# Performance work log

Hardware: AMD Instinct MI355X
Metric: run time of the kernel (lower is better)

The kernel has to match this reference:

```python
import jax, jax.numpy as jnp
import numpy as np

RING_SIZES = list(range(3, 27, 2))  # 3,5,...,25 -> 12 rings; (1+12)*96 = 1248
BN_EPS = 1e-5


def _box_sum(x, k):
    """Sum over k x k window (k odd), 'same' zero padding. x: [B,C,H,W].
    O(1) per pixel via summed-area table instead of dense depthwise conv."""
    p = k // 2
    H, W = x.shape[2], x.shape[3]
    xp = jnp.pad(x, ((0, 0), (0, 0), (p, p), (p, p)))
    S = jnp.cumsum(jnp.cumsum(xp, axis=2), axis=3)
    S = jnp.pad(S, ((0, 0), (0, 0), (1, 0), (1, 0)))  # leading zero row/col
    return (S[:, :, k:k + H, k:k + W] - S[:, :, :H, k:k + W]
            - S[:, :, k:k + H, :W] + S[:, :, :H, :W])


def _ring_sum(x, k):
    """Depthwise conv with a k x k ring of ones == box(k) - box(k-2)."""
    inner = x if k == 3 else _box_sum(x, k - 2)
    return _box_sum(x, k) - inner


def _bn_eval(x, gamma, beta, mean, var):
    scale = gamma / jnp.sqrt(var + BN_EPS)
    return x * scale[None, :, None, None] + (beta - mean * scale)[None, :, None, None]


def _conv1x1(x, w, b):
    # x: [B,C,H,W], w: [O,C] -> [B,O,H,W]
    return jnp.einsum('bchw,oc->bohw', x, w) + b[None, :, None, None]


def setup_inputs() -> dict:
    key = jax.random.key(0)
    ks = jax.random.split(key, 13)
    B, C, H, W = 4, 96, 128, 128
    return {
        'x': jax.random.normal(ks[0], (B, C, H, W), jnp.float32),
        'bn1_gamma': jax.random.uniform(ks[1], (1248,), jnp.float32, 0.5, 1.5),
        'bn1_beta': jax.random.normal(ks[2], (1248,), jnp.float32) * 0.1,
        'bn1_mean': jax.random.normal(ks[3], (1248,), jnp.float32),
        'bn1_var': jax.random.uniform(ks[4], (1248,), jnp.float32, 0.5, 1.5),
        'conv1_w': jax.random.normal(ks[5], (512, 1248), jnp.float32) * (1.0 / np.sqrt(1248)),
        'conv1_b': jax.random.normal(ks[6], (512,), jnp.float32) * 0.01,
        'bn2_gamma': jax.random.uniform(ks[7], (512,), jnp.float32, 0.5, 1.5),
        'bn2_beta': jax.random.normal(ks[8], (512,), jnp.float32) * 0.1,
        'bn2_mean': jax.random.normal(ks[9], (512,), jnp.float32),
        'bn2_var': jax.random.uniform(ks[10], (512,), jnp.float32, 0.5, 1.5),
        'conv2_w': jax.random.normal(ks[11], (96, 512), jnp.float32) * (1.0 / np.sqrt(512)),
        'conv2_b': jax.random.normal(ks[12], (96,), jnp.float32) * 0.01,
    }


def reference(x, bn1_gamma, bn1_beta, bn1_mean, bn1_var, conv1_w, conv1_b,
              bn2_gamma, bn2_beta, bn2_mean, bn2_var, conv2_w, conv2_b):
    convs = [x] + [_ring_sum(x, k) for k in RING_SIZES]
    h = jnp.concatenate(convs, axis=1)  # [B, 1248, H, W]
    h = _bn_eval(h, bn1_gamma, bn1_beta, bn1_mean, bn1_var)
    h = jax.nn.relu(_conv1x1(h, conv1_w, conv1_b))
    h = _bn_eval(h, bn2_gamma, bn2_beta, bn2_mean, bn2_var)
    return _conv1x1(h, conv2_w, conv2_b)
```

## Files before the change

### kernel.cpp

```cpp
#include <hip/hip_runtime.h>
#include <hip/hip_bf16.h>
#include <cstdint>

typedef __attribute__((ext_vector_type(8))) short bf16x8;
typedef __attribute__((ext_vector_type(4))) float f32x4;

#define BN_EPS 1e-5f

__global__ __launch_bounds__(256) void prep1_kernel(
    const float* __restrict__ W1, const float* __restrict__ cb1,
    const float* __restrict__ g1, const float* __restrict__ be1,
    const float* __restrict__ mu1, const float* __restrict__ va1,
    __hip_bfloat16* __restrict__ V, float* __restrict__ b1e)
{
  int o = blockIdx.x;
  int t = threadIdx.x;
  const float* wrow = W1 + (size_t)o * 1248;
  float acc = 0.f;
  for (int i = t; i < 1248; i += 256) {
    float s = g1[i] * rsqrtf(va1[i] + BN_EPS);
    float w = wrow[i];
    acc += w * (be1[i] - mu1[i] * s);
    float g = w * s;
    float gn = 0.f;
    if (i < 1152) {
      float sn = g1[i + 96] * rsqrtf(va1[i + 96] + BN_EPS);
      gn = wrow[i + 96] * sn;
    }
    V[(size_t)o * 1248 + i] = __float2bfloat16(g - gn);
  }
  for (int d = 32; d > 0; d >>= 1) acc += __shfl_down(acc, d);
  __shared__ float red[4];
  int lane = t & 63, wv = t >> 6;
  if (lane == 0) red[wv] = acc;
  __syncthreads();
  if (t == 0) b1e[o] = cb1[o] + red[0] + red[1] + red[2] + red[3];
}

__global__ __launch_bounds__(256) void prep2_kernel(
    const float* __restrict__ W2, const float* __restrict__ cb2,
    const float* __restrict__ g2, const float* __restrict__ be2,
    const float* __restrict__ mu2, const float* __restrict__ va2,
    __hip_bfloat16* __restrict__ W2e, float* __restrict__ b2e)
{
  int o = blockIdx.x;
  int t = threadIdx.x;
  const float* wrow = W2 + (size_t)o * 512;
  float acc = 0.f;
  for (int j = t; j < 512; j += 256) {
    float s = g2[j] * rsqrtf(va2[j] + BN_EPS);
    float wv = wrow[j];
    acc += wv * (be2[j] - mu2[j] * s);
    W2e[(size_t)o * 512 + j] = __float2bfloat16(wv * s);
  }
  for (int d = 32; d > 0; d >>= 1) acc += __shfl_down(acc, d);
  __shared__ float red[4];
  int lane = t & 63, wv2 = t >> 6;
  if (lane == 0) red[wv2] = acc;
  __syncthreads();
  if (t == 0) b2e[o] = cb2[o] + red[0] + red[1] + red[2] + red[3];
}

__global__ __launch_bounds__(128) void sat_kernel(
    const float* __restrict__ x, float* __restrict__ SAT)
{
  int plane = blockIdx.x;
  const float* xp = x + (size_t)plane * 16384;
  __shared__ float tile[16384];
  int t = threadIdx.x;
  for (int i4 = t; i4 < 4096; i4 += 128) {
    int r = i4 >> 5;
    int g = i4 & 31;
    float4 v = *(const float4*)(xp + (size_t)r * 128 + g * 4);
    *(float4*)(tile + r * 128 + ((g ^ (r & 31)) << 2)) = v;
  }
  __syncthreads();
  {
    int r = t;
    float carry = 0.f;
    for (int g = 0; g < 32; ++g) {
      float* p = tile + r * 128 + ((g ^ (r & 31)) << 2);
      float4 v = *(float4*)p;
      float s0 = carry + v.x, s1 = s0 + v.y, s2 = s1 + v.z, s3 = s2 + v.w;
      float4 o; o.x = s0; o.y = s1; o.z = s2; o.w = s3;
      *(float4*)p = o;
      carry = s3;
    }
  }
  __syncthreads();
  float* Sg = SAT + (size_t)plane * 17028;
  Sg[t] = 0.f;
  if (t < 4) Sg[128 + t] = 0.f;
  Sg[(t + 1) * 132] = 0.f;
  int gc = t >> 2, wc = t & 3;
  float run = 0.f;
  for (int r = 0; r < 128; ++r) {
    run += tile[r * 128 + ((gc ^ (r & 31)) << 2) + wc];
    Sg[(r + 1) * 132 + t + 1] = run;
  }
}

__global__ __launch_bounds__(1024) void fused1_kernel(
    const float* __restrict__ SAT, const __hip_bfloat16* __restrict__ V,
    const float* __restrict__ b1e, const __hip_bfloat16* __restrict__ W2e,
    const float* __restrict__ b2e, float* __restrict__ out, int nb, int b0)
{
  extern __shared__ __align__(16) char smem[];
  float* E = (float*)smem;
  __hip_bfloat16* As = (__hip_bfloat16*)(smem + 50688);

  int blk = blockIdx.x;
  int rows_per_xcd = (nb * 128) >> 3;
  int r = (blk & 7) * rows_per_xcd + (blk >> 3);
  int bL = r >> 7, y = r & 127;

  int t = threadIdx.x;
  int lane = t & 63, wv = t >> 6;
  int wm = wv & 1, wn = wv >> 1;
  int lr = lane & 15, quad = lane >> 4;
  int px = t & 127;
  int bg = t >> 7;

  const float* Sb = SAT + (size_t)bL * 96 * 17028;

  f32x4 acc[4][4];
#pragma unroll
  for (int i = 0; i < 4; ++i)
#pragma unroll
    for (int jn = 0; jn < 4; ++jn) acc[i][jn] = (f32x4){0.f, 0.f, 0.f, 0.f};

  auto efill = [&](int j) {
    int y1 = (y - j < 0) ? 0 : (y - j);
    int y2 = ((y + j > 127) ? 127 : (y + j)) + 1;
    for (int idx = t; idx < 3168; idx += 1024) {
      int cl = idx / 33;
      int ck = idx - cl * 33;
      const float* bp = Sb + (size_t)cl * 17028 + ck * 4;
      float4 a = *(const float4*)(bp + y2 * 132);
      float4 b = *(const float4*)(bp + y1 * 132);
      float4 d;
      d.x = a.x - b.x; d.y = a.y - b.y; d.z = a.z - b.z; d.w = a.w - b.w;
      *(float4*)(E + cl * 132 + ck * 4) = d;
    }
  };

  efill(0);
  __syncthreads();

  for (int j = 0; j < 13; ++j) {
    int x1 = (px - j < 0) ? 0 : (px - j);
    int x2 = ((px + j > 127) ? 127 : (px + j)) + 1;
    {
      const float* Eb = E + bg * 8 * 132;
      union { bf16x8 v; __hip_bfloat16 h[8]; } pk;
#pragma unroll
      for (int i = 0; i < 8; ++i)
        pk.h[i] = __float2bfloat16(Eb[i * 132 + x2] - Eb[i * 132 + x1]);
      *(bf16x8*)(As + px * 104 + bg * 8) = pk.v;
      if (bg < 4) {
        const float* Eb2 = E + (8 + bg) * 8 * 132;
        union { bf16x8 v; __hip_bfloat16 h[8]; } pk2;
#pragma unroll
        for (int i = 0; i < 8; ++i)
          pk2.h[i] = __float2bfloat16(Eb2[i * 132 + x2] - Eb2[i * 132 + x1]);
        *(bf16x8*)(As + px * 104 + (8 + bg) * 8) = pk2.v;
      }
    }
    __syncthreads();

#pragma unroll
    for (int sub = 0; sub < 3; ++sub) {
      bf16x8 af[4], bfr[4];
#pragma unroll
      for (int i = 0; i < 4; ++i)
        af[i] = *(const bf16x8*)(As + (wm * 64 + i * 16 + lr) * 104 + sub * 32 + quad * 8);
#pragma unroll
      for (int jn = 0; jn < 4; ++jn)
        bfr[jn] = *(const bf16x8*)(V + (size_t)(wn * 64 + jn * 16 + lr) * 1248
                                   + j * 96 + sub * 32 + quad * 8);
#pragma unroll
      for (int i = 0; i < 4; ++i)
#pragma unroll
        for (int jn = 0; jn < 4; ++jn)
          acc[i][jn] = __builtin_amdgcn_mfma_f32_16x16x32_bf16(af[i], bfr[jn], acc[i][jn], 0, 0, 0);
      if (sub == 0 && j < 12) efill(j + 1);
    }
    __syncthreads();
  }

  __hip_bfloat16* Yst = (__hip_bfloat16*)smem;
#pragma unroll
  for (int jn = 0; jn < 4; ++jn) {
    int n = wn * 64 + jn * 16 + lr;
    float bias = b1e[n];
#pragma unroll
    for (int i = 0; i < 4; ++i) {
#pragma unroll
      for (int rr = 0; rr < 4; ++rr) {
        int m = wm * 64 + i * 16 + quad * 4 + rr;
        float z = acc[i][jn][rr] + bias;
        z = z > 0.f ? z : 0.f;
        Yst[m * 520 + n] = __float2bfloat16(z);
      }
    }
  }
  __syncthreads();

  int pxt = wv & 7;
  int mh = wv >> 3;
  f32x4 acc2[3];
#pragma unroll
  for (int im = 0; im < 3; ++im) acc2[im] = (f32x4){0.f, 0.f, 0.f, 0.f};

  for (int k2 = 0; k2 < 512; k2 += 32) {
    bf16x8 bfr2 = *(const bf16x8*)(Yst + (pxt * 16 + lr) * 520 + k2 + quad * 8);
#pragma unroll
    for (int im = 0; im < 3; ++im) {
      bf16x8 afr2 = *(const bf16x8*)(W2e + (size_t)(mh * 48 + im * 16 + lr) * 512
                                     + k2 + quad * 8);
      acc2[im] = __builtin_amdgcn_mfma_f32_16x16x32_bf16(afr2, bfr2, acc2[im], 0, 0, 0);
    }
  }

  size_t obase = ((size_t)(b0 + bL) * 96) * 16384 + (size_t)y * 128 + pxt * 16 + lr;
#pragma unroll
  for (int im = 0; im < 3; ++im) {
#pragma unroll
    for (int rr = 0; rr < 4; ++rr) {
      int o2 = mh * 48 + im * 16 + quad * 4 + rr;
      out[obase + (size_t)o2 * 16384] = acc2[im][rr] + b2e[o2];
    }
  }
}

extern "C" void kernel_launch(void* const* d_in, const int* in_sizes, int n_in,
                              void* d_out, int out_size, void* d_ws, size_t ws_size,
                              hipStream_t stream)
{
  const float* x   = (const float*)d_in[0];
  const float* g1  = (const float*)d_in[1];
  const float* be1 = (const float*)d_in[2];
  const float* mu1 = (const float*)d_in[3];
  const float* va1 = (const float*)d_in[4];
  const float* W1  = (const float*)d_in[5];
  const float* cb1 = (const float*)d_in[6];
  const float* g2  = (const float*)d_in[7];
  const float* be2 = (const float*)d_in[8];
  const float* mu2 = (const float*)d_in[9];
  const float* va2 = (const float*)d_in[10];
  const float* W2  = (const float*)d_in[11];
  const float* cb2 = (const float*)d_in[12];
  float* out = (float*)d_out;

  hipFuncSetAttribute((const void*)fused1_kernel,
                      hipFuncAttributeMaxDynamicSharedMemorySize, 133120);

  char* w = (char*)d_ws;
  __hip_bfloat16* V   = (__hip_bfloat16*)w; w += (size_t)512 * 1248 * 2;
  __hip_bfloat16* W2e = (__hip_bfloat16*)w; w += (size_t)96 * 512 * 2;
  float* b1e = (float*)w; w += 2048;
  float* b2e = (float*)w; w += 512;
  size_t fixed = (size_t)(w - (char*)d_ws);

  const size_t satB = (size_t)96 * 17028 * 4;
  int nb = (ws_size >= fixed + 4 * satB + 4096) ? 4 : 1;

  float* SAT = (float*)w;

  prep1_kernel<<<512, 256, 0, stream>>>(W1, cb1, g1, be1, mu1, va1, V, b1e);
  prep2_kernel<<<96, 256, 0, stream>>>(W2, cb2, g2, be2, mu2, va2, W2e, b2e);

  for (int b0 = 0; b0 < 4; b0 += nb) {
    sat_kernel<<<nb * 96, 128, 0, stream>>>(x + (size_t)b0 * 96 * 16384, SAT);
    fused1_kernel<<<nb * 128, 1024, 133120, stream>>>(SAT, V, b1e, W2e, b2e, out, nb, b0);
  }
}
```

Baseline: 305.6 us.

## Double-buffer ring stages with wave-specialized overlap and parallelize SAT scan

The fused kernel now keeps two E buffers and two A-tile buffers, so the row-difference fill and bf16 tile build for the next rings run alongside the MFMA work for the current ring. Odd and even waves run the compute and fill phases in opposite order, and s_setprio raises wave priority during MFMA. One barrier per ring replaces two. The SAT kernel goes from 128 to 512 threads, splitting each prefix scan into four chunks joined by per-chunk offsets. Costs: more shared memory per block (about 151 KB), which may limit occupancy, plus extra offset passes in the SAT kernel.

```diff
diff --git a/kernel.cpp b/kernel.cpp
--- a/kernel.cpp
+++ b/kernel.cpp
@@ -61,24 +61,30 @@
   if (t == 0) b2e[o] = cb2[o] + red[0] + red[1] + red[2] + red[3];
 }
 
-__global__ __launch_bounds__(128) void sat_kernel(
+__global__ __launch_bounds__(512) void sat_kernel(
     const float* __restrict__ x, float* __restrict__ SAT)
 {
   int plane = blockIdx.x;
   const float* xp = x + (size_t)plane * 16384;
   __shared__ float tile[16384];
+  __shared__ float csA[128 * 4];
+  __shared__ float csB[128 * 4];
   int t = threadIdx.x;
-  for (int i4 = t; i4 < 4096; i4 += 128) {
+
+  for (int i4 = t; i4 < 4096; i4 += 512) {
     int r = i4 >> 5;
     int g = i4 & 31;
     float4 v = *(const float4*)(xp + (size_t)r * 128 + g * 4);
     *(float4*)(tile + r * 128 + ((g ^ (r & 31)) << 2)) = v;
   }
   __syncthreads();
+
+  int r = t & 127, ch = t >> 7;
   {
-    int r = t;
     float carry = 0.f;
-    for (int g = 0; g < 32; ++g) {
+#pragma unroll
+    for (int g8 = 0; g8 < 8; ++g8) {
+      int g = ch * 8 + g8;
       float* p = tile + r * 128 + ((g ^ (r & 31)) << 2);
       float4 v = *(float4*)p;
       float s0 = carry + v.x, s1 = s0 + v.y, s2 = s1 + v.z, s3 = s2 + v.w;
@@ -86,17 +92,50 @@
       *(float4*)p = o;
       carry = s3;
     }
-  }
-  __syncthreads();
+    csA[r * 4 + ch] = carry;
+  }
+  __syncthreads();
+  if (ch > 0) {
+    float offs = csA[r * 4 + 0];
+    if (ch > 1) offs += csA[r * 4 + 1];
+    if (ch > 2) offs += csA[r * 4 + 2];
+#pragma unroll
+    for (int g8 = 0; g8 < 8; ++g8) {
+      int g = ch * 8 + g8;
+      float* p = tile + r * 128 + ((g ^ (r & 31)) << 2);
+      float4 v = *(float4*)p;
+      v.x += offs; v.y += offs; v.z += offs; v.w += offs;
+      *(float4*)p = v;
+    }
+  }
+  __syncthreads();
+
   float* Sg = SAT + (size_t)plane * 17028;
-  Sg[t] = 0.f;
-  if (t < 4) Sg[128 + t] = 0.f;
-  Sg[(t + 1) * 132] = 0.f;
-  int gc = t >> 2, wc = t & 3;
-  float run = 0.f;
-  for (int r = 0; r < 128; ++r) {
-    run += tile[r * 128 + ((gc ^ (r & 31)) << 2) + wc];
-    Sg[(r + 1) * 132 + t + 1] = run;
+  int xcol = t & 127, rc = t >> 7;
+  int gc = xcol >> 2, wc = xcol & 3;
+  float regs[32];
+  {
+    float run = 0.f;
+#pragma unroll
+    for (int r8 = 0; r8 < 32; ++r8) {
+      int rr = rc * 32 + r8;
+      run += tile[rr * 128 + ((gc ^ (rr & 31)) << 2) + wc];
+      regs[r8] = run;
+    }
+    csB[xcol * 4 + rc] = run;
+  }
+  if (t < 132) Sg[t] = 0.f;
+  if (t < 128) Sg[(t + 1) * 132] = 0.f;
+  __syncthreads();
+
+  float offs = 0.f;
+  if (rc > 0) offs += csB[xcol * 4 + 0];
+  if (rc > 1) offs += csB[xcol * 4 + 1];
+  if (rc > 2) offs += csB[xcol * 4 + 2];
+#pragma unroll
+  for (int r8 = 0; r8 < 32; ++r8) {
+    int rr = rc * 32 + r8;
+    Sg[(rr + 1) * 132 + xcol + 1] = regs[r8] + offs;
   }
 }
 
@@ -106,8 +145,10 @@
     const float* __restrict__ b2e, float* __restrict__ out, int nb, int b0)
 {
   extern __shared__ __align__(16) char smem[];
-  float* E = (float*)smem;
-  __hip_bfloat16* As = (__hip_bfloat16*)(smem + 50688);
+  float* E0 = (float*)smem;
+  float* E1 = (float*)(smem + 50688);
+  __hip_bfloat16* As0 = (__hip_bfloat16*)(smem + 101376);
+  __hip_bfloat16* As1 = (__hip_bfloat16*)(smem + 128000);
 
   int blk = blockIdx.x;
   int rows_per_xcd = (nb * 128) >> 3;
@@ -129,9 +170,9 @@
 #pragma unroll
     for (int jn = 0; jn < 4; ++jn) acc[i][jn] = (f32x4){0.f, 0.f, 0.f, 0.f};
 
-  auto efill = [&](int j) {
-    int y1 = (y - j < 0) ? 0 : (y - j);
-    int y2 = ((y + j > 127) ? 127 : (y + j)) + 1;
+  auto efill = [&](float* E, int jr) {
+    int y1 = (y - jr < 0) ? 0 : (y - jr);
+    int y2 = ((y + jr > 127) ? 127 : (y + jr)) + 1;
     for (int idx = t; idx < 3168; idx += 1024) {
       int cl = idx / 33;
       int ck = idx - cl * 33;
@@ -144,30 +185,27 @@
     }
   };
 
-  efill(0);
-  __syncthreads();
-
-  for (int j = 0; j < 13; ++j) {
-    int x1 = (px - j < 0) ? 0 : (px - j);
-    int x2 = ((px + j > 127) ? 127 : (px + j)) + 1;
-    {
-      const float* Eb = E + bg * 8 * 132;
-      union { bf16x8 v; __hip_bfloat16 h[8]; } pk;
+  auto build = [&](__hip_bfloat16* As, const float* E, int jr) {
+    int x1 = (px - jr < 0) ? 0 : (px - jr);
+    int x2 = ((px + jr > 127) ? 127 : (px + jr)) + 1;
+    const float* Eb = E + bg * 8 * 132;
+    union { bf16x8 v; __hip_bfloat16 h[8]; } pk;
+#pragma unroll
+    for (int i = 0; i < 8; ++i)
+      pk.h[i] = __float2bfloat16(Eb[i * 132 + x2] - Eb[i * 132 + x1]);
+    *(bf16x8*)(As + px * 104 + bg * 8) = pk.v;
+    if (bg < 4) {
+      const float* Eb2 = E + (8 + bg) * 8 * 132;
+      union { bf16x8 v; __hip_bfloat16 h[8]; } pk2;
 #pragma unroll
       for (int i = 0; i < 8; ++i)
-        pk.h[i] = __float2bfloat16(Eb[i * 132 + x2] - Eb[i * 132 + x1]);
-      *(bf16x8*)(As + px * 104 + bg * 8) = pk.v;
-      if (bg < 4) {
-        const float* Eb2 = E + (8 + bg) * 8 * 132;
-        union { bf16x8 v; __hip_bfloat16 h[8]; } pk2;
-#pragma unroll
-        for (int i = 0; i < 8; ++i)
-          pk2.h[i] = __float2bfloat16(Eb2[i * 132 + x2] - Eb2[i * 132 + x1]);
-        *(bf16x8*)(As + px * 104 + (8 + bg) * 8) = pk2.v;
-      }
-    }
-    __syncthreads();
-
+        pk2.h[i] = __float2bfloat16(Eb2[i * 132 + x2] - Eb2[i * 132 + x1]);
+      *(bf16x8*)(As + px * 104 + (8 + bg) * 8) = pk2.v;
+    }
+  };
+
+  auto mfma_ring = [&](int j, const __hip_bfloat16* As) {
+    __builtin_amdgcn_s_setprio(1);
 #pragma unroll
     for (int sub = 0; sub < 3; ++sub) {
       bf16x8 af[4], bfr[4];
@@ -183,9 +221,33 @@
 #pragma unroll
         for (int jn = 0; jn < 4; ++jn)
           acc[i][jn] = __builtin_amdgcn_mfma_f32_16x16x32_bf16(af[i], bfr[jn], acc[i][jn], 0, 0, 0);
-      if (sub == 0 && j < 12) efill(j + 1);
+    }
+    __builtin_amdgcn_s_setprio(0);
+  };
+
+  auto ring_iter = [&](int j, const float* Esrc, float* Edst,
+                       const __hip_bfloat16* Asrc, __hip_bfloat16* Adst) {
+    if (wv & 1) {
+      mfma_ring(j, Asrc);
+      if (j < 11) efill(Edst, j + 2);
+      if (j < 12) build(Adst, Esrc, j + 1);
+    } else {
+      if (j < 11) efill(Edst, j + 2);
+      if (j < 12) build(Adst, Esrc, j + 1);
+      mfma_ring(j, Asrc);
     }
     __syncthreads();
+  };
+
+  efill(E0, 0);
+  __syncthreads();
+  efill(E1, 1);
+  build(As0, E0, 0);
+  __syncthreads();
+
+  for (int j = 0; j < 13; j += 2) {
+    ring_iter(j, E1, E0, As0, As1);
+    if (j + 1 < 13) ring_iter(j + 1, E0, E1, As1, As0);
   }
 
   __hip_bfloat16* Yst = (__hip_bfloat16*)smem;
@@ -253,7 +315,7 @@
   float* out = (float*)d_out;
 
   hipFuncSetAttribute((const void*)fused1_kernel,
-                      hipFuncAttributeMaxDynamicSharedMemorySize, 133120);
+                      hipFuncAttributeMaxDynamicSharedMemorySize, 154624);
 
   char* w = (char*)d_ws;
   __hip_bfloat16* V   = (__hip_bfloat16*)w; w += (size_t)512 * 1248 * 2;
@@ -271,7 +333,7 @@
   prep2_kernel<<<96, 256, 0, stream>>>(W2, cb2, g2, be2, mu2, va2, W2e, b2e);
 
   for (int b0 = 0; b0 < 4; b0 += nb) {
-    sat_kernel<<<nb * 96, 128, 0, stream>>>(x + (size_t)b0 * 96 * 16384, SAT);
-    fused1_kernel<<<nb * 128, 1024, 133120, stream>>>(SAT, V, b1e, W2e, b2e, out, nb, b0);
-  }
-}
+    sat_kernel<<<nb * 96, 512, 0, stream>>>(x + (size_t)b0 * 96 * 16384, SAT);
+    fused1_kernel<<<nb * 128, 1024, 154624, stream>>>(SAT, V, b1e, W2e, b2e, out, nb, b0);
+  }
+}
```

After: 302.4 us. Within noise of the previous version (-1.1%).
